# Kernel tuning notes

Measured on AMD Instinct MI355X. Metric: run time of the kernel, lower is better.

## Reference

```python
import jax, jax.numpy as jnp
import numpy as np

B, S, H = 2, 2048, 1024
NH, NKV, HD = 16, 4, 64
Q_SIZE = NH * HD          # 1024
KV_SIZE = NKV * HD        # 256
R_SOFTPLUS_0 = 1.442695041
NEG = -2.3819763e38  # large negative for masking (matches float32 -inf-ish additive mask)


def setup_inputs() -> dict:
    key = jax.random.key(0)
    k1, k2, k3, k4, k5, k6 = jax.random.split(key, 6)
    hidden_states = jax.random.normal(k1, (B, S, H), dtype=jnp.float32)
    # causal additive mask [B, 1, S, S]
    causal = jnp.tril(jnp.ones((S, S), dtype=bool))
    mask = jnp.where(causal, 0.0, NEG).astype(jnp.float32)
    mask = jnp.broadcast_to(mask[None, None], (B, 1, S, S))
    fan = 1.0 / np.sqrt(H)
    qkv_w = jax.random.uniform(k2, ((NH + 2 * NKV) * HD, H), jnp.float32, -fan, fan)
    qkv_b = jax.random.uniform(k3, ((NH + 2 * NKV) * HD,), jnp.float32, -fan, fan)
    fo = 1.0 / np.sqrt(Q_SIZE)
    o_w = jax.random.uniform(k4, (H, Q_SIZE), jnp.float32, -fo, fo)
    o_b = jax.random.uniform(k5, (H,), jnp.float32, -fo, fo)
    scaling = jax.random.normal(k6, (HD,), dtype=jnp.float32)
    return {"hidden_states": hidden_states, "mask": mask, "scaling": scaling,
            "qkv_w": qkv_w, "qkv_b": qkv_b, "o_w": o_w, "o_b": o_b}


def reference(hidden_states, mask, scaling, qkv_w, qkv_b, o_w, o_b):
    b, s, _ = hidden_states.shape
    q_w, k_w, v_w = qkv_w[:Q_SIZE], qkv_w[Q_SIZE:Q_SIZE + KV_SIZE], qkv_w[-KV_SIZE:]
    q_b, k_b, v_b = qkv_b[:Q_SIZE], qkv_b[Q_SIZE:Q_SIZE + KV_SIZE], qkv_b[-KV_SIZE:]
    xq = (hidden_states @ q_w.T + q_b).reshape(b, s, NH, HD)
    # per-dim softplus scaling fused into q
    scale = (R_SOFTPLUS_0 / np.sqrt(HD)) * jax.nn.softplus(scaling)
    xq = xq * scale[None, None, None, :]
    xk = (hidden_states @ k_w.T + k_b).reshape(b, s, NKV, HD)
    xv = (hidden_states @ v_w.T + v_b).reshape(b, s, NKV, HD)
    # GQA: repeat kv heads (repeat_interleave along head dim)
    key = jnp.repeat(xk, NH // NKV, axis=2)   # [b, s, NH, HD]
    value = jnp.repeat(xv, NH // NKV, axis=2)
    scores = jnp.einsum('bqhd,bkhd->bhqk', xq, key) + mask
    scores = jax.nn.softmax(scores.astype(jnp.float32), axis=-1).astype(xq.dtype)
    out = jnp.einsum('bhqk,bkhd->bqhd', scores, value).reshape(b, s, NH * HD)
    out = out @ o_w.T + o_b
    return scores, out
```

## Files before the change

### kernel.cpp

```cpp
#include <hip/hip_runtime.h>
#include <hip/hip_bf16.h>
#include <cstdint>
#include <cstddef>

typedef __attribute__((ext_vector_type(4))) float f32x4;
typedef __attribute__((ext_vector_type(8))) short bf16x8;

#define DEVI static __device__ __forceinline__

DEVI unsigned short f2bf(float f) {
  union { float f; unsigned int u; } v; v.f = f;
  unsigned int u = v.u;
  unsigned int r = (u + 0x7fffu + ((u >> 16) & 1u)) >> 16;
  return (unsigned short)r;
}

DEVI unsigned int cvt_pk(float lo, float hi) {
  unsigned int r;
  asm("v_cvt_pk_bf16_f32 %0, %1, %2" : "=v"(r) : "v"(lo), "v"(hi));
  return r;
}

DEVI f32x4 mfma16(bf16x8 a, bf16x8 b, f32x4 c) {
  return __builtin_amdgcn_mfma_f32_16x16x32_bf16(a, b, c, 0, 0, 0);
}

#define GLDS(gp, lp) __builtin_amdgcn_global_load_lds(                         \
    (const __attribute__((address_space(1))) void*)(const void*)(gp),          \
    (__attribute__((address_space(3))) void*)(void*)(lp), 16, 0, 0)

#define SBAR() asm volatile("s_barrier" ::: "memory")
#define WV(n) asm volatile("s_waitcnt vmcnt(" #n ")" ::: "memory")
#define FORCE4(x) asm volatile("" : "+v"(x))

__global__ void convert_kernel(const float* __restrict__ hidden,
                               const float* __restrict__ qkv_w,
                               const float* __restrict__ o_w,
                               const float* __restrict__ scaling,
                               unsigned short* __restrict__ hbf,
                               unsigned short* __restrict__ wbf,
                               unsigned short* __restrict__ obf,
                               float* __restrict__ qscale) {
  int tid = blockIdx.x * blockDim.x + threadIdx.x;
  int nt = gridDim.x * blockDim.x;
  if (tid < 64) {
    float x = scaling[tid];
    float sp = (x > 20.f) ? x : log1pf(__expf(x));
    qscale[tid] = 0.1803368801243369f * 1.4426950408889634f * sp;
  }
  for (int i = tid; i < 1048576; i += nt) {
    float4 v = ((const float4*)hidden)[i];
    ushort4 o = { f2bf(v.x), f2bf(v.y), f2bf(v.z), f2bf(v.w) };
    ((ushort4*)hbf)[i] = o;
  }
  for (int i = tid; i < 393216; i += nt) {
    float4 v = ((const float4*)qkv_w)[i];
    ushort4 o = { f2bf(v.x), f2bf(v.y), f2bf(v.z), f2bf(v.w) };
    ((ushort4*)wbf)[i] = o;
  }
  for (int i = tid; i < 262144; i += nt) {
    float4 v = ((const float4*)o_w)[i];
    ushort4 o = { f2bf(v.x), f2bf(v.y), f2bf(v.z), f2bf(v.w) };
    ((ushort4*)obf)[i] = o;
  }
}

template <int EPI>
__global__ __launch_bounds__(256, 2) void gemm_kernel(
    const unsigned short* __restrict__ A,
    const unsigned short* __restrict__ Bw,
    const float* __restrict__ bias,
    const float* __restrict__ qscale,
    unsigned short* __restrict__ oq,
    unsigned short* __restrict__ okv,
    unsigned short* __restrict__ ovt,
    float* __restrict__ of) {
  __shared__ __align__(16) unsigned short sA[128 * 64];
  __shared__ __align__(16) unsigned short sB[128 * 64];
  const int t = threadIdx.x, lane = t & 63, w = t >> 6;
  const int l15 = lane & 15, lg = lane >> 4;
  const int m0 = blockIdx.y * 128, n0 = blockIdx.x * 128;
  const int wr = w >> 1, wc = w & 1;

  f32x4 acc[4][4] = {};

  for (int kb = 0; kb < 1024; kb += 64) {
    __syncthreads();
#pragma unroll
    for (int i = 0; i < 4; i++) {
      int idx = i * 256 + w * 64 + lane;
      int row = idx >> 3;
      int cg = (idx & 7) ^ (row & 7);
      GLDS(A + (size_t)(m0 + row) * 1024 + kb + cg * 8, sA + (i * 256 + w * 64) * 8);
      GLDS(Bw + (size_t)(n0 + row) * 1024 + kb + cg * 8, sB + (i * 256 + w * 64) * 8);
    }
    __syncthreads();
    bf16x8 af[4][2], bfr[4][2];
#pragma unroll
    for (int rt = 0; rt < 4; rt++) {
      int row = wr * 64 + rt * 16 + l15;
#pragma unroll
      for (int kk = 0; kk < 2; kk++) {
        int c = (kk * 4 + lg) ^ (row & 7);
        af[rt][kk] = *(const bf16x8*)((const char*)sA + row * 128 + c * 16);
      }
      int rowb = wc * 64 + rt * 16 + l15;
#pragma unroll
      for (int kk = 0; kk < 2; kk++) {
        int c = (kk * 4 + lg) ^ (rowb & 7);
        bfr[rt][kk] = *(const bf16x8*)((const char*)sB + rowb * 128 + c * 16);
      }
    }
#pragma unroll
    for (int kk = 0; kk < 2; kk++)
#pragma unroll
      for (int rt = 0; rt < 4; rt++)
#pragma unroll
        for (int ct = 0; ct < 4; ct++)
          acc[rt][ct] = mfma16(af[rt][kk], bfr[ct][kk], acc[rt][ct]);
  }

#pragma unroll
  for (int rt = 0; rt < 4; rt++) {
#pragma unroll
    for (int ct = 0; ct < 4; ct++) {
      int n = n0 + wc * 64 + ct * 16 + l15;
      float bv = bias[n];
#pragma unroll
      for (int jj = 0; jj < 4; jj++) {
        int m = m0 + wr * 64 + rt * 16 + lg * 4 + jj;
        float v = acc[rt][ct][jj] + bv;
        if (EPI == 1) {
          int b = m >> 11, s = m & 2047;
          if (n < 1024) {
            int h = n >> 6, d = n & 63;
            v *= qscale[d];
            oq[(((size_t)(b * 16 + h) * 2048 + s) << 6) + d] = f2bf(v);
          } else if (n < 1280) {
            int kv = (n - 1024) >> 6, d = n & 63;
            okv[(((size_t)(b * 4 + kv) * 2048 + s) << 6) + d] = f2bf(v);
          } else {
            int kv = (n - 1280) >> 6, d = n & 63;
            ovt[(((size_t)((b * 4 + kv) * 64 + d)) << 11) + s] = f2bf(v);
          }
        } else {
          of[(size_t)m * 1024 + n] = v;
        }
      }
    }
  }
}

__global__ __launch_bounds__(256, 2) void attn_kernel(
    const unsigned short* __restrict__ q_ws,
    const unsigned short* __restrict__ k_ws,
    const unsigned short* __restrict__ v_ws,
    float* __restrict__ scores,
    unsigned short* __restrict__ attn_bf) {
  __shared__ __align__(16) unsigned short sK[2][4096];
  __shared__ __align__(16) unsigned short sVT[2][4096];
  __shared__ __align__(16) unsigned char sP[4][2048];

  const int t = threadIdx.x, lane = t & 63, w = t >> 6;
  const int l15 = lane & 15, lg = lane >> 4;
  int bid = blockIdx.x;
  int bh = bid & 31;
  int p = bid >> 5;
  int b = bh >> 4, h = bh & 15, kv = h >> 2;
  const int qtA = p, qtB = 31 - p;
  const int NB = qtB + 1;

  const unsigned short* Kp = k_ws + ((size_t)(b * 4 + kv) * 2048) * 64;
  const unsigned short* Vp = v_ws + ((size_t)(b * 4 + kv) * 64) * 2048;
  const int qrA = qtA * 64 + w * 16 + l15;
  const int qrB = qtB * 64 + w * 16 + l15;

  bf16x8 aqA[2], aqB[2];
  {
    const unsigned short* qa = q_ws + ((size_t)bh * 2048 + qrA) * 64;
    const unsigned short* qb = q_ws + ((size_t)bh * 2048 + qrB) * 64;
    aqA[0] = *(const bf16x8*)(qa + lg * 8);
    aqA[1] = *(const bf16x8*)(qa + 32 + lg * 8);
    aqB[0] = *(const bf16x8*)(qb + lg * 8);
    aqB[1] = *(const bf16x8*)(qb + 32 + lg * 8);
    FORCE4(*(f32x4*)&aqA[0]); FORCE4(*(f32x4*)&aqA[1]);
    FORCE4(*(f32x4*)&aqB[0]); FORCE4(*(f32x4*)&aqB[1]);
  }

  auto stageK = [&](int kt, int bufi) {
#pragma unroll
    for (int i = 0; i < 2; i++) {
      int idx = i * 256 + w * 64 + lane;
      int row = idx >> 3;
      int cg = (idx & 7) ^ (row & 7);
      GLDS(Kp + (size_t)(kt * 64 + row) * 64 + cg * 8, sK[bufi] + (i * 256 + w * 64) * 8);
    }
  };
  auto stageVT = [&](int kt, int bufi) {
#pragma unroll
    for (int i = 0; i < 2; i++) {
      int idx = i * 256 + w * 64 + lane;
      int row = idx >> 3;
      int cg = (idx & 7) ^ (row & 7);
      GLDS(Vp + (size_t)row * 2048 + kt * 64 + cg * 8, sVT[bufi] + (i * 256 + w * 64) * 8);
    }
  };
  auto qk_tile = [&](const unsigned short* kb, const bf16x8(&aq)[2], f32x4(&acc)[4]) {
#pragma unroll
    for (int ct = 0; ct < 4; ct++) {
      int row = ct * 16 + l15;
#pragma unroll
      for (int kk = 0; kk < 2; kk++) {
        int c = (kk * 4 + lg) ^ (row & 7);
        bf16x8 ak = *(const bf16x8*)((const char*)kb + row * 128 + c * 16);
        acc[ct] = mfma16(ak, aq[kk], acc[ct]);
      }
    }
  };

  stageK(0, 0);
  float rsA = 0.f, rsB = 0.f;
  for (int n = 0; n < NB; n++) {
    if (n + 1 < NB) { stageK(n + 1, (n + 1) & 1); WV(2); } else { WV(0); }
    SBAR();
    const unsigned short* kb = sK[n & 1];
    {
      f32x4 acc[4] = {};
      qk_tile(kb, aqB, acc);
      if (n < NB - 1) {
#pragma unroll
        for (int ct = 0; ct < 4; ct++)
#pragma unroll
          for (int j = 0; j < 4; j++) rsB += __builtin_amdgcn_exp2f(acc[ct][j]);
      } else {
#pragma unroll
        for (int ct = 0; ct < 4; ct++) {
          int kb0 = n * 64 + ct * 16 + lg * 4;
#pragma unroll
          for (int j = 0; j < 4; j++)
            rsB += (kb0 + j <= qrB) ? __builtin_amdgcn_exp2f(acc[ct][j]) : 0.f;
        }
      }
    }
    if (n <= qtA) {
      f32x4 acc[4] = {};
      qk_tile(kb, aqA, acc);
      if (n < qtA) {
#pragma unroll
        for (int ct = 0; ct < 4; ct++)
#pragma unroll
          for (int j = 0; j < 4; j++) rsA += __builtin_amdgcn_exp2f(acc[ct][j]);
      } else {
#pragma unroll
        for (int ct = 0; ct < 4; ct++) {
          int kb0 = n * 64 + ct * 16 + lg * 4;
#pragma unroll
          for (int j = 0; j < 4; j++)
            rsA += (kb0 + j <= qrA) ? __builtin_amdgcn_exp2f(acc[ct][j]) : 0.f;
        }
      }
    }
    SBAR();
  }
  rsA += __shfl_xor(rsA, 16); rsA += __shfl_xor(rsA, 32);
  rsB += __shfl_xor(rsB, 16); rsB += __shfl_xor(rsB, 32);
  float rinvA = 1.0f / rsA, rinvB = 1.0f / rsB;

  stageK(0, 0); stageVT(0, 0);
  f32x4 accoA[4] = {}, accoB[4] = {};
  unsigned char* myP = &sP[w][0];
  const int xr = (l15 & 7) << 4;
  float* SpA = scores + ((size_t)bh * 2048 + qtA * 64) * 2048;
  float* SpB = scores + ((size_t)bh * 2048 + qtB * 64) * 2048;

  for (int n = 0; n < NB; n++) {
    if (n + 1 < NB) { stageK(n + 1, (n + 1) & 1); stageVT(n + 1, (n + 1) & 1); }
    if (n == 0) { WV(4); } else if (n + 1 < NB) { WV(12); } else { WV(8); }
    SBAR();
    const unsigned short* kb = sK[n & 1];
    const unsigned short* vt = sVT[n & 1];
    int k0 = n * 64;

    {
      f32x4 acc[4] = {};
      qk_tile(kb, aqB, acc);
      if (n == NB - 1) {
#pragma unroll
        for (int ct = 0; ct < 4; ct++) {
          int kb0 = k0 + ct * 16 + lg * 4;
#pragma unroll
          for (int j = 0; j < 4; j++)
            acc[ct][j] = (kb0 + j <= qrB) ? __builtin_amdgcn_exp2f(acc[ct][j]) * rinvB : 0.f;
        }
      } else {
#pragma unroll
        for (int ct = 0; ct < 4; ct++)
#pragma unroll
          for (int j = 0; j < 4; j++)
            acc[ct][j] = __builtin_amdgcn_exp2f(acc[ct][j]) * rinvB;
      }
      float* srow = SpB + (size_t)(w * 16 + l15) * 2048 + k0 + lg * 4;
#pragma unroll
      for (int ct = 0; ct < 4; ct++) *(f32x4*)(srow + ct * 16) = acc[ct];
#pragma unroll
      for (int ct = 0; ct < 4; ct++) {
        uint2 pw;
        pw.x = cvt_pk(acc[ct][0], acc[ct][1]);
        pw.y = cvt_pk(acc[ct][2], acc[ct][3]);
        *(uint2*)(myP + l15 * 128 + ((ct * 32 + lg * 8) ^ xr)) = pw;
      }
#pragma unroll
      for (int kk = 0; kk < 2; kk++) {
        bf16x8 ap = *(const bf16x8*)(myP + l15 * 128 + ((kk * 64 + lg * 16) ^ xr));
#pragma unroll
        for (int ct = 0; ct < 4; ct++) {
          int vrow = ct * 16 + l15;
          int cv = (kk * 4 + lg) ^ (vrow & 7);
          bf16x8 bv = *(const bf16x8*)((const char*)vt + vrow * 128 + cv * 16);
          accoB[ct] = mfma16(bv, ap, accoB[ct]);
        }
      }
    }

    if (n <= qtA) {
      f32x4 acc[4] = {};
      qk_tile(kb, aqA, acc);
      if (n == qtA) {
#pragma unroll
        for (int ct = 0; ct < 4; ct++) {
          int kb0 = k0 + ct * 16 + lg * 4;
#pragma unroll
          for (int j = 0; j < 4; j++)
            acc[ct][j] = (kb0 + j <= qrA) ? __builtin_amdgcn_exp2f(acc[ct][j]) * rinvA : 0.f;
        }
      } else {
#pragma unroll
        for (int ct = 0; ct < 4; ct++)
#pragma unroll
          for (int j = 0; j < 4; j++)
            acc[ct][j] = __builtin_amdgcn_exp2f(acc[ct][j]) * rinvA;
      }
      float* srow = SpA + (size_t)(w * 16 + l15) * 2048 + k0 + lg * 4;
#pragma unroll
      for (int ct = 0; ct < 4; ct++) *(f32x4*)(srow + ct * 16) = acc[ct];
#pragma unroll
      for (int ct = 0; ct < 4; ct++) {
        uint2 pw;
        pw.x = cvt_pk(acc[ct][0], acc[ct][1]);
        pw.y = cvt_pk(acc[ct][2], acc[ct][3]);
        *(uint2*)(myP + l15 * 128 + ((ct * 32 + lg * 8) ^ xr)) = pw;
      }
#pragma unroll
      for (int kk = 0; kk < 2; kk++) {
        bf16x8 ap = *(const bf16x8*)(myP + l15 * 128 + ((kk * 64 + lg * 16) ^ xr));
#pragma unroll
        for (int ct = 0; ct < 4; ct++) {
          int vrow = ct * 16 + l15;
          int cv = (kk * 4 + lg) ^ (vrow & 7);
          bf16x8 bv = *(const bf16x8*)((const char*)vt + vrow * 128 + cv * 16);
          accoA[ct] = mfma16(bv, ap, accoA[ct]);
        }
      }
    } else {
      f32x4 z = {0.f, 0.f, 0.f, 0.f};
      float* srow = SpA + (size_t)(w * 16 + l15) * 2048 + k0 + lg * 4;
#pragma unroll
      for (int ct = 0; ct < 4; ct++) *(f32x4*)(srow + ct * 16) = z;
    }
    SBAR();
  }

  {
    int mA = b * 2048 + qtA * 64 + w * 16 + l15;
    int mB = b * 2048 + qtB * 64 + w * 16 + l15;
    unsigned int* oA = (unsigned int*)(attn_bf + (size_t)mA * 1024 + h * 64);
    unsigned int* oB = (unsigned int*)(attn_bf + (size_t)mB * 1024 + h * 64);
#pragma unroll
    for (int ct = 0; ct < 4; ct++) {
      uint2 pa, pb;
      pa.x = cvt_pk(accoA[ct][0], accoA[ct][1]);
      pa.y = cvt_pk(accoA[ct][2], accoA[ct][3]);
      pb.x = cvt_pk(accoB[ct][0], accoB[ct][1]);
      pb.y = cvt_pk(accoB[ct][2], accoB[ct][3]);
      *(uint2*)(oA + (ct * 16 + lg * 4) / 2) = pa;
      *(uint2*)(oB + (ct * 16 + lg * 4) / 2) = pb;
    }
  }

  int zbase = NB * 64;
  if (zbase < 2048) {
    f32x4 z = {0.f, 0.f, 0.f, 0.f};
    float* ra = scores + ((size_t)bh * 2048 + qrA) * 2048;
    float* rb = scores + ((size_t)bh * 2048 + qrB) * 2048;
    for (int c = zbase + lg * 4; c < 2048; c += 16) {
      *(f32x4*)(ra + c) = z;
      *(f32x4*)(rb + c) = z;
    }
  }
}

extern "C" void kernel_launch(void* const* d_in, const int* in_sizes, int n_in,
                              void* d_out, int out_size, void* d_ws, size_t ws_size,
                              hipStream_t stream) {
  const float* hidden  = (const float*)d_in[0];
  const float* scaling = (const float*)d_in[2];
  const float* qkv_w   = (const float*)d_in[3];
  const float* qkv_b   = (const float*)d_in[4];
  const float* o_w     = (const float*)d_in[5];
  const float* o_b     = (const float*)d_in[6];

  float* scores = (float*)d_out;
  float* outp   = (float*)d_out + (size_t)2 * 16 * 2048 * 2048;

  char* ws = (char*)d_ws;
  unsigned short* hidden_bf = (unsigned short*)(ws + 0);
  unsigned short* qkvw_bf   = (unsigned short*)(ws + 8388608);
  unsigned short* ow_bf     = (unsigned short*)(ws + 11534336);
  unsigned short* q_ws      = (unsigned short*)(ws + 13631488);
  unsigned short* k_ws      = (unsigned short*)(ws + 22020096);
  unsigned short* v_ws      = (unsigned short*)(ws + 24117248);
  unsigned short* attn_bf   = (unsigned short*)(ws + 26214400);
  float* qscale             = (float*)(ws + 34603008);

  convert_kernel<<<512, 256, 0, stream>>>(hidden, qkv_w, o_w, scaling,
                                          hidden_bf, qkvw_bf, ow_bf, qscale);
  gemm_kernel<1><<<dim3(12, 32), 256, 0, stream>>>(hidden_bf, qkvw_bf, qkv_b,
                                                   qscale, q_ws, k_ws, v_ws, nullptr);
  attn_kernel<<<512, 256, 0, stream>>>(q_ws, k_ws, v_ws, scores, attn_bf);
  gemm_kernel<2><<<dim3(8, 32), 256, 0, stream>>>(attn_bf, ow_bf, o_b, nullptr,
                                                  nullptr, nullptr, nullptr, outp);
}
```

Baseline: 216.8 us.

## Interleave A/B QK and PV MFMAs, move zero-fill into pass one, use nontemporal stores

The attention kernel now computes the QK tiles for both query tiles (A and B) from each shared K fragment in one interleaved loop. The PV products likewise share each V fragment, with the P scratch split into separate per-tile buffers. The masked-region zero writes for the scores move out of the second pass and the tail loop into the first (row-sum) pass as nontemporal stores, and score and output stores also use nontemporal hints. Wait-count thresholds are adjusted to match the new number of outstanding memory operations. The aim is more independent MFMA chains per LDS load and overlap of the large zero-fill traffic with compute, at the cost of more registers and twice the LDS for P.

```diff
diff --git a/kernel.cpp b/kernel.cpp
--- a/kernel.cpp
+++ b/kernel.cpp
@@ -144,7 +144,7 @@
             ovt[(((size_t)((b * 4 + kv) * 64 + d)) << 11) + s] = f2bf(v);
           }
         } else {
-          of[(size_t)m * 1024 + n] = v;
+          __builtin_nontemporal_store(v, &of[(size_t)m * 1024 + n]);
         }
       }
     }
@@ -159,7 +159,7 @@
     unsigned short* __restrict__ attn_bf) {
   __shared__ __align__(16) unsigned short sK[2][4096];
   __shared__ __align__(16) unsigned short sVT[2][4096];
-  __shared__ __align__(16) unsigned char sP[4][2048];
+  __shared__ __align__(16) unsigned char sP[8][2048];
 
   const int t = threadIdx.x, lane = t & 63, w = t >> 6;
   const int l15 = lane & 15, lg = lane >> 4;
@@ -218,48 +218,80 @@
     }
   };
 
+  auto zstore = [&](int zi) {
+    int zc = (zi < 31 - p) ? (p + 1 + zi) : (zi + 1);
+    int rt = (zi < 31 - p) ? qtA : qtB;
+    float* rowp = scores + ((size_t)bh * 2048 + rt * 64 + w * 16 + l15) * 2048
+                  + zc * 64 + lg * 4;
+    f32x4 z = {0.f, 0.f, 0.f, 0.f};
+#pragma unroll
+    for (int ct = 0; ct < 4; ct++)
+      __builtin_nontemporal_store(z, (f32x4*)(rowp + ct * 16));
+  };
+
   stageK(0, 0);
   float rsA = 0.f, rsB = 0.f;
   for (int n = 0; n < NB; n++) {
-    if (n + 1 < NB) { stageK(n + 1, (n + 1) & 1); WV(2); } else { WV(0); }
+    if (n + 1 < NB) {
+      stageK(n + 1, (n + 1) & 1);
+      if (n == 0) { WV(2); }
+      else if (n <= 15) { WV(10); }
+      else if (n == 16) { WV(6); }
+      else { WV(2); }
+    } else {
+      if (n == 16) { WV(4); } else { WV(0); }
+    }
     SBAR();
     const unsigned short* kb = sK[n & 1];
-    {
-      f32x4 acc[4] = {};
-      qk_tile(kb, aqB, acc);
-      if (n < NB - 1) {
+    bool doA = (n <= qtA);
+    f32x4 aB[4] = {};
+    if (doA) {
+      f32x4 aA[4] = {};
+#pragma unroll
+      for (int ct = 0; ct < 4; ct++) {
+        int row = ct * 16 + l15;
+#pragma unroll
+        for (int kk = 0; kk < 2; kk++) {
+          int c = (kk * 4 + lg) ^ (row & 7);
+          bf16x8 ak = *(const bf16x8*)((const char*)kb + row * 128 + c * 16);
+          aB[ct] = mfma16(ak, aqB[kk], aB[ct]);
+          aA[ct] = mfma16(ak, aqA[kk], aA[ct]);
+        }
+      }
+      if (n < qtA) {
 #pragma unroll
         for (int ct = 0; ct < 4; ct++)
 #pragma unroll
-          for (int j = 0; j < 4; j++) rsB += __builtin_amdgcn_exp2f(acc[ct][j]);
+          for (int j = 0; j < 4; j++) rsA += __builtin_amdgcn_exp2f(aA[ct][j]);
       } else {
 #pragma unroll
         for (int ct = 0; ct < 4; ct++) {
           int kb0 = n * 64 + ct * 16 + lg * 4;
 #pragma unroll
           for (int j = 0; j < 4; j++)
-            rsB += (kb0 + j <= qrB) ? __builtin_amdgcn_exp2f(acc[ct][j]) : 0.f;
-        }
-      }
-    }
-    if (n <= qtA) {
-      f32x4 acc[4] = {};
-      qk_tile(kb, aqA, acc);
-      if (n < qtA) {
-#pragma unroll
-        for (int ct = 0; ct < 4; ct++)
-#pragma unroll
-          for (int j = 0; j < 4; j++) rsA += __builtin_amdgcn_exp2f(acc[ct][j]);
-      } else {
-#pragma unroll
-        for (int ct = 0; ct < 4; ct++) {
-          int kb0 = n * 64 + ct * 16 + lg * 4;
-#pragma unroll
-          for (int j = 0; j < 4; j++)
-            rsA += (kb0 + j <= qrA) ? __builtin_amdgcn_exp2f(acc[ct][j]) : 0.f;
-        }
-      }
-    }
+            rsA += (kb0 + j <= qrA) ? __builtin_amdgcn_exp2f(aA[ct][j]) : 0.f;
+        }
+      }
+    } else {
+      qk_tile(kb, aqB, aB);
+    }
+    if (n < NB - 1) {
+#pragma unroll
+      for (int ct = 0; ct < 4; ct++)
+#pragma unroll
+        for (int j = 0; j < 4; j++) rsB += __builtin_amdgcn_exp2f(aB[ct][j]);
+    } else {
+#pragma unroll
+      for (int ct = 0; ct < 4; ct++) {
+        int kb0 = n * 64 + ct * 16 + lg * 4;
+#pragma unroll
+        for (int j = 0; j < 4; j++)
+          rsB += (kb0 + j <= qrB) ? __builtin_amdgcn_exp2f(aB[ct][j]) : 0.f;
+      }
+    }
+    int zi0 = 2 * n;
+    if (zi0 < 31) zstore(zi0);
+    if (zi0 + 1 < 31) zstore(zi0 + 1);
     SBAR();
   }
   rsA += __shfl_xor(rsA, 16); rsA += __shfl_xor(rsA, 32);
@@ -268,104 +300,124 @@
 
   stageK(0, 0); stageVT(0, 0);
   f32x4 accoA[4] = {}, accoB[4] = {};
-  unsigned char* myP = &sP[w][0];
+  unsigned char* myPB = &sP[w][0];
+  unsigned char* myPA = &sP[4 + w][0];
   const int xr = (l15 & 7) << 4;
   float* SpA = scores + ((size_t)bh * 2048 + qtA * 64) * 2048;
   float* SpB = scores + ((size_t)bh * 2048 + qtB * 64) * 2048;
 
   for (int n = 0; n < NB; n++) {
+    bool doA = (n <= qtA);
     if (n + 1 < NB) { stageK(n + 1, (n + 1) & 1); stageVT(n + 1, (n + 1) & 1); }
-    if (n == 0) { WV(4); } else if (n + 1 < NB) { WV(12); } else { WV(8); }
+    if (n == 0) { WV(4); }
+    else if (n + 1 < NB) { if (n - 1 <= qtA) { WV(12); } else { WV(8); } }
+    else { if (n - 1 <= qtA) { WV(8); } else { WV(4); } }
     SBAR();
     const unsigned short* kb = sK[n & 1];
     const unsigned short* vt = sVT[n & 1];
     int k0 = n * 64;
 
+    f32x4 aB[4] = {}, aA[4] = {};
+    if (doA) {
+#pragma unroll
+      for (int ct = 0; ct < 4; ct++) {
+        int row = ct * 16 + l15;
+#pragma unroll
+        for (int kk = 0; kk < 2; kk++) {
+          int c = (kk * 4 + lg) ^ (row & 7);
+          bf16x8 ak = *(const bf16x8*)((const char*)kb + row * 128 + c * 16);
+          aB[ct] = mfma16(ak, aqB[kk], aB[ct]);
+          aA[ct] = mfma16(ak, aqA[kk], aA[ct]);
+        }
+      }
+    } else {
+      qk_tile(kb, aqB, aB);
+    }
+
+    if (n == NB - 1) {
+#pragma unroll
+      for (int ct = 0; ct < 4; ct++) {
+        int kb0 = k0 + ct * 16 + lg * 4;
+#pragma unroll
+        for (int j = 0; j < 4; j++)
+          aB[ct][j] = (kb0 + j <= qrB) ? __builtin_amdgcn_exp2f(aB[ct][j]) * rinvB : 0.f;
+      }
+    } else {
+#pragma unroll
+      for (int ct = 0; ct < 4; ct++)
+#pragma unroll
+        for (int j = 0; j < 4; j++)
+          aB[ct][j] = __builtin_amdgcn_exp2f(aB[ct][j]) * rinvB;
+    }
     {
-      f32x4 acc[4] = {};
-      qk_tile(kb, aqB, acc);
-      if (n == NB - 1) {
+      float* srow = SpB + (size_t)(w * 16 + l15) * 2048 + k0 + lg * 4;
+#pragma unroll
+      for (int ct = 0; ct < 4; ct++)
+        __builtin_nontemporal_store(aB[ct], (f32x4*)(srow + ct * 16));
+#pragma unroll
+      for (int ct = 0; ct < 4; ct++) {
+        uint2 pw;
+        pw.x = cvt_pk(aB[ct][0], aB[ct][1]);
+        pw.y = cvt_pk(aB[ct][2], aB[ct][3]);
+        *(uint2*)(myPB + l15 * 128 + ((ct * 32 + lg * 8) ^ xr)) = pw;
+      }
+    }
+
+    if (doA) {
+      if (n == qtA) {
 #pragma unroll
         for (int ct = 0; ct < 4; ct++) {
           int kb0 = k0 + ct * 16 + lg * 4;
 #pragma unroll
           for (int j = 0; j < 4; j++)
-            acc[ct][j] = (kb0 + j <= qrB) ? __builtin_amdgcn_exp2f(acc[ct][j]) * rinvB : 0.f;
+            aA[ct][j] = (kb0 + j <= qrA) ? __builtin_amdgcn_exp2f(aA[ct][j]) * rinvA : 0.f;
         }
       } else {
 #pragma unroll
         for (int ct = 0; ct < 4; ct++)
 #pragma unroll
           for (int j = 0; j < 4; j++)
-            acc[ct][j] = __builtin_amdgcn_exp2f(acc[ct][j]) * rinvB;
-      }
-      float* srow = SpB + (size_t)(w * 16 + l15) * 2048 + k0 + lg * 4;
-#pragma unroll
-      for (int ct = 0; ct < 4; ct++) *(f32x4*)(srow + ct * 16) = acc[ct];
+            aA[ct][j] = __builtin_amdgcn_exp2f(aA[ct][j]) * rinvA;
+      }
+      float* srow = SpA + (size_t)(w * 16 + l15) * 2048 + k0 + lg * 4;
+#pragma unroll
+      for (int ct = 0; ct < 4; ct++)
+        __builtin_nontemporal_store(aA[ct], (f32x4*)(srow + ct * 16));
 #pragma unroll
       for (int ct = 0; ct < 4; ct++) {
         uint2 pw;
-        pw.x = cvt_pk(acc[ct][0], acc[ct][1]);
-        pw.y = cvt_pk(acc[ct][2], acc[ct][3]);
-        *(uint2*)(myP + l15 * 128 + ((ct * 32 + lg * 8) ^ xr)) = pw;
-      }
+        pw.x = cvt_pk(aA[ct][0], aA[ct][1]);
+        pw.y = cvt_pk(aA[ct][2], aA[ct][3]);
+        *(uint2*)(myPA + l15 * 128 + ((ct * 32 + lg * 8) ^ xr)) = pw;
+      }
+    }
+
+    if (doA) {
 #pragma unroll
       for (int kk = 0; kk < 2; kk++) {
-        bf16x8 ap = *(const bf16x8*)(myP + l15 * 128 + ((kk * 64 + lg * 16) ^ xr));
+        bf16x8 apB = *(const bf16x8*)(myPB + l15 * 128 + ((kk * 64 + lg * 16) ^ xr));
+        bf16x8 apA = *(const bf16x8*)(myPA + l15 * 128 + ((kk * 64 + lg * 16) ^ xr));
 #pragma unroll
         for (int ct = 0; ct < 4; ct++) {
           int vrow = ct * 16 + l15;
           int cv = (kk * 4 + lg) ^ (vrow & 7);
           bf16x8 bv = *(const bf16x8*)((const char*)vt + vrow * 128 + cv * 16);
-          accoB[ct] = mfma16(bv, ap, accoB[ct]);
-        }
-      }
-    }
-
-    if (n <= qtA) {
-      f32x4 acc[4] = {};
-      qk_tile(kb, aqA, acc);
-      if (n == qtA) {
-#pragma unroll
-        for (int ct = 0; ct < 4; ct++) {
-          int kb0 = k0 + ct * 16 + lg * 4;
-#pragma unroll
-          for (int j = 0; j < 4; j++)
-            acc[ct][j] = (kb0 + j <= qrA) ? __builtin_amdgcn_exp2f(acc[ct][j]) * rinvA : 0.f;
-        }
-      } else {
-#pragma unroll
-        for (int ct = 0; ct < 4; ct++)
-#pragma unroll
-          for (int j = 0; j < 4; j++)
-            acc[ct][j] = __builtin_amdgcn_exp2f(acc[ct][j]) * rinvA;
-      }
-      float* srow = SpA + (size_t)(w * 16 + l15) * 2048 + k0 + lg * 4;
-#pragma unroll
-      for (int ct = 0; ct < 4; ct++) *(f32x4*)(srow + ct * 16) = acc[ct];
-#pragma unroll
-      for (int ct = 0; ct < 4; ct++) {
-        uint2 pw;
-        pw.x = cvt_pk(acc[ct][0], acc[ct][1]);
-        pw.y = cvt_pk(acc[ct][2], acc[ct][3]);
-        *(uint2*)(myP + l15 * 128 + ((ct * 32 + lg * 8) ^ xr)) = pw;
-      }
+          accoB[ct] = mfma16(bv, apB, accoB[ct]);
+          accoA[ct] = mfma16(bv, apA, accoA[ct]);
+        }
+      }
+    } else {
 #pragma unroll
       for (int kk = 0; kk < 2; kk++) {
-        bf16x8 ap = *(const bf16x8*)(myP + l15 * 128 + ((kk * 64 + lg * 16) ^ xr));
+        bf16x8 apB = *(const bf16x8*)(myPB + l15 * 128 + ((kk * 64 + lg * 16) ^ xr));
 #pragma unroll
         for (int ct = 0; ct < 4; ct++) {
           int vrow = ct * 16 + l15;
           int cv = (kk * 4 + lg) ^ (vrow & 7);
           bf16x8 bv = *(const bf16x8*)((const char*)vt + vrow * 128 + cv * 16);
-          accoA[ct] = mfma16(bv, ap, accoA[ct]);
-        }
-      }
-    } else {
-      f32x4 z = {0.f, 0.f, 0.f, 0.f};
-      float* srow = SpA + (size_t)(w * 16 + l15) * 2048 + k0 + lg * 4;
-#pragma unroll
-      for (int ct = 0; ct < 4; ct++) *(f32x4*)(srow + ct * 16) = z;
+          accoB[ct] = mfma16(bv, apB, accoB[ct]);
+        }
+      }
     }
     SBAR();
   }
@@ -384,17 +436,6 @@
       pb.y = cvt_pk(accoB[ct][2], accoB[ct][3]);
       *(uint2*)(oA + (ct * 16 + lg * 4) / 2) = pa;
       *(uint2*)(oB + (ct * 16 + lg * 4) / 2) = pb;
-    }
-  }
-
-  int zbase = NB * 64;
-  if (zbase < 2048) {
-    f32x4 z = {0.f, 0.f, 0.f, 0.f};
-    float* ra = scores + ((size_t)bh * 2048 + qrA) * 2048;
-    float* rb = scores + ((size_t)bh * 2048 + qrB) * 2048;
-    for (int c = zbase + lg * 4; c < 2048; c += 16) {
-      *(f32x4*)(ra + c) = z;
-      *(f32x4*)(rb + c) = z;
     }
   }
 }
```

After: 283.9 us. +31.0%, slower.

## Move upper-triangle zero stores into the row-sum pass to overlap with compute

Applied to the files above, without the earlier changes.

The zero-filling of masked score tiles is moved out of the second pass and the kernel tail and into the first (row-sum) pass, two tiles per iteration. The goal is to hide those global stores behind the QK MFMA work of the first pass instead of serialising them at the end. The vmcnt wait counts in both loops are retuned to match the extra outstanding stores. The hand-tuned wait counts depend on the paired-tile indexing (p, qtA, qtB), so a miscount could cause a hazard or an unnecessary stall.

```diff
diff --git a/kernel.cpp b/kernel.cpp
--- a/kernel.cpp
+++ b/kernel.cpp
@@ -218,10 +218,29 @@
     }
   };
 
+  auto zstore = [&](int zi) {
+    int zc = (zi < 31 - p) ? (p + 1 + zi) : (zi + 1);
+    int rt = (zi < 31 - p) ? qtA : qtB;
+    float* rowp = scores + ((size_t)bh * 2048 + rt * 64 + w * 16 + l15) * 2048
+                  + zc * 64 + lg * 4;
+    f32x4 z = {0.f, 0.f, 0.f, 0.f};
+#pragma unroll
+    for (int ct = 0; ct < 4; ct++)
+      *(f32x4*)(rowp + ct * 16) = z;
+  };
+
   stageK(0, 0);
   float rsA = 0.f, rsB = 0.f;
   for (int n = 0; n < NB; n++) {
-    if (n + 1 < NB) { stageK(n + 1, (n + 1) & 1); WV(2); } else { WV(0); }
+    if (n + 1 < NB) {
+      stageK(n + 1, (n + 1) & 1);
+      if (n == 0) { WV(2); }
+      else if (n <= 15) { WV(10); }
+      else if (n == 16) { WV(6); }
+      else { WV(2); }
+    } else {
+      if (n == 16) { WV(4); } else { WV(0); }
+    }
     SBAR();
     const unsigned short* kb = sK[n & 1];
     {
@@ -260,6 +279,9 @@
         }
       }
     }
+    int zi0 = 2 * n;
+    if (zi0 < 31) zstore(zi0);
+    if (zi0 + 1 < 31) zstore(zi0 + 1);
     SBAR();
   }
   rsA += __shfl_xor(rsA, 16); rsA += __shfl_xor(rsA, 32);
@@ -275,7 +297,9 @@
 
   for (int n = 0; n < NB; n++) {
     if (n + 1 < NB) { stageK(n + 1, (n + 1) & 1); stageVT(n + 1, (n + 1) & 1); }
-    if (n == 0) { WV(4); } else if (n + 1 < NB) { WV(12); } else { WV(8); }
+    if (n == 0) { WV(4); }
+    else if (n + 1 < NB) { if (n - 1 <= qtA) { WV(12); } else { WV(8); } }
+    else { if (n - 1 <= qtA) { WV(8); } else { WV(4); } }
     SBAR();
     const unsigned short* kb = sK[n & 1];
     const unsigned short* vt = sVT[n & 1];
@@ -361,11 +385,6 @@
           accoA[ct] = mfma16(bv, ap, accoA[ct]);
         }
       }
-    } else {
-      f32x4 z = {0.f, 0.f, 0.f, 0.f};
-      float* srow = SpA + (size_t)(w * 16 + l15) * 2048 + k0 + lg * 4;
-#pragma unroll
-      for (int ct = 0; ct < 4; ct++) *(f32x4*)(srow + ct * 16) = z;
     }
     SBAR();
   }
@@ -384,17 +403,6 @@
       pb.y = cvt_pk(accoB[ct][2], accoB[ct][3]);
       *(uint2*)(oA + (ct * 16 + lg * 4) / 2) = pa;
       *(uint2*)(oB + (ct * 16 + lg * 4) / 2) = pb;
-    }
-  }
-
-  int zbase = NB * 64;
-  if (zbase < 2048) {
-    f32x4 z = {0.f, 0.f, 0.f, 0.f};
-    float* ra = scores + ((size_t)bh * 2048 + qrA) * 2048;
-    float* rb = scores + ((size_t)bh * 2048 + qrB) * 2048;
-    for (int c = zbase + lg * 4; c < 2048; c += 16) {
-      *(f32x4*)(ra + c) = z;
-      *(f32x4*)(rb + c) = z;
     }
   }
 }
```

Result: slower. 221.4 us (+2.1%).
